# Optimization experiments

Hardware: AMD Instinct MI355X
Metric: run time of the kernel (lower is better)

Reference implementation:

```python
import jax, jax.numpy as jnp
import numpy as np

HIDDEN = 1024
HEADS = 16
HEAD_DIM = HIDDEN // HEADS  # 64
BATCH = 2
SEQ = 2048
MASK_IDENTITY = True


def setup_inputs() -> dict:
    key = jax.random.key(0)
    ks = jax.random.split(key, 9)
    s = 1.0 / np.sqrt(HIDDEN)
    return {
        "hidden_states": jax.random.normal(ks[0], (BATCH, SEQ, HIDDEN), jnp.float32),
        "Wq": jax.random.normal(ks[1], (HIDDEN, HIDDEN), jnp.float32) * s,
        "bq": jnp.zeros((HIDDEN,), jnp.float32),
        "Wk": jax.random.normal(ks[2], (HIDDEN, HIDDEN), jnp.float32) * s,
        "bk": jnp.zeros((HIDDEN,), jnp.float32),
        "Wv": jax.random.normal(ks[3], (HIDDEN, HIDDEN), jnp.float32) * s,
        "bv": jnp.zeros((HIDDEN,), jnp.float32),
        "Wd": jax.random.normal(ks[4], (HIDDEN, HIDDEN), jnp.float32) * s,
        "bd": jnp.zeros((HIDDEN,), jnp.float32),
    }


def _split_heads(x):
    # [B, S, H*Dh] -> [B, H, S, Dh]
    b, s, _ = x.shape
    return x.reshape(b, s, HEADS, HEAD_DIM).transpose(0, 2, 1, 3)


def reference(hidden_states, Wq, bq, Wk, bk, Wv, bv, Wd, bd):
    # torch Linear: y = x @ W.T + b
    q = _split_heads(hidden_states @ Wq.T + bq)  # [B,H,S,Dh]
    k = _split_heads(hidden_states @ Wk.T + bk)
    v = _split_heads(hidden_states @ Wv.T + bv)

    scores = jnp.einsum("bhqd,bhkd->bhqk", q, k) / np.sqrt(HEAD_DIM)
    if MASK_IDENTITY:
        mask_value = -jnp.finfo(scores.dtype).max
        eye = jnp.eye(scores.shape[-1], dtype=bool)  # [S,S], broadcast over B,H
        scores = jnp.where(eye, mask_value, scores)
    probs = jax.nn.softmax(scores, axis=-1)
    ctx = jnp.einsum("bhqk,bhkd->bhqd", probs, v)  # [B,H,S,Dh]
    b, h, s, d = ctx.shape
    ctx = ctx.transpose(0, 2, 1, 3).reshape(b, s, h * d)  # [B,S,H*Dh]
    return ctx @ Wd.T + bd
```

## Files before the change

kernel.cpp:

```cpp
#include <hip/hip_runtime.h>
#include <hip/hip_bf16.h>
#include <stdint.h>

#define HIDDEN 1024
#define SEQL   2048
#define NB     2
#define NH     16
#define DH     64
#define MTOT   (NB * SEQL)
#define QKVLD  3072
#define SCALE_Q 0.18033688011112042f

typedef __bf16 bf16x8 __attribute__((ext_vector_type(8)));
typedef __bf16 bf16x4 __attribute__((ext_vector_type(4)));
typedef float  f32x4  __attribute__((ext_vector_type(4)));
typedef float  f32x16 __attribute__((ext_vector_type(16)));

__device__ __forceinline__ void gload16(const void* g, void* l) {
    __builtin_amdgcn_global_load_lds(
        (const __attribute__((address_space(1))) void*)g,
        (__attribute__((address_space(3))) void*)l, 16, 0, 0);
}
__device__ __forceinline__ float exp2fast(float x) {
    float r;
    asm("v_exp_f32 %0, %1" : "=v"(r) : "v"(x));
    return r;
}
__device__ __forceinline__ unsigned cvtpk(float lo, float hi) {
    unsigned r;
    asm("v_cvt_pk_bf16_f32 %0, %1, %2" : "=v"(r) : "v"(lo), "v"(hi));
    return r;
}
__device__ __forceinline__ void pswap(unsigned& a, unsigned& b) {
    asm volatile("v_permlane32_swap_b32 %0, %1" : "+v"(a), "+v"(b));
}
__device__ __forceinline__ void barrier_vm3() {
    asm volatile("s_waitcnt vmcnt(3)" ::: "memory");
    __builtin_amdgcn_s_barrier();
    asm volatile("" ::: "memory");
}
__device__ __forceinline__ void barrier_vm4() {
    asm volatile("s_waitcnt vmcnt(4)" ::: "memory");
    __builtin_amdgcn_s_barrier();
    asm volatile("" ::: "memory");
}

__global__ void prep(const float* __restrict__ H,
                     const float* __restrict__ Wq, const float* __restrict__ Wk,
                     const float* __restrict__ Wv, const float* __restrict__ Wd,
                     const float* __restrict__ bq, const float* __restrict__ bk,
                     const float* __restrict__ bv,
                     __bf16* __restrict__ Hb, __bf16* __restrict__ Wall,
                     float* __restrict__ bqkv) {
    const int bid = blockIdx.x, tid = threadIdx.x;
    if (bid < 4096) {
        int i = bid * 256 + tid;
        float4 v = reinterpret_cast<const float4*>(H)[i];
        bf16x4 o = { (__bf16)v.x, (__bf16)v.y, (__bf16)v.z, (__bf16)v.w };
        reinterpret_cast<bf16x4*>(Hb)[i] = o;
    } else if (bid < 8192) {
        int wi = bid - 4096;
        int seg = wi >> 10;
        int i = (wi & 1023) * 256 + tid;
        const float* src = seg == 0 ? Wq : seg == 1 ? Wk : seg == 2 ? Wv : Wd;
        float sc = (seg == 0) ? SCALE_Q : 1.0f;
        float4 v = reinterpret_cast<const float4*>(src)[i];
        bf16x4 o = { (__bf16)(v.x * sc), (__bf16)(v.y * sc),
                     (__bf16)(v.z * sc), (__bf16)(v.w * sc) };
        reinterpret_cast<bf16x4*>(Wall)[(size_t)seg * 262144 + i] = o;
    } else {
        for (int i = tid; i < 3072; i += 256) {
            float v = (i < 1024) ? bq[i] * SCALE_Q
                    : (i < 2048) ? bk[i - 1024] : bv[i - 2048];
            bqkv[i] = v;
        }
    }
}

__global__ __launch_bounds__(256) void transpose_v(const __bf16* __restrict__ QKV,
                                                   __bf16* __restrict__ Vt) {
    __shared__ __bf16 t[64][66];
    const int st = blockIdx.x, bh = blockIdx.y;
    const int b = bh >> 4, h = bh & 15;
    const int tid = threadIdx.x;
    const int r = tid >> 3, c = tid & 7;
    const __bf16* src = QKV + (size_t)(b * SEQL + st * 64) * QKVLD + 2048 + h * 64;
    *(int4*)&t[r][c * 8]      = *(const int4*)(src + (size_t)r * QKVLD + c * 8);
    *(int4*)&t[r + 32][c * 8] = *(const int4*)(src + (size_t)(r + 32) * QKVLD + c * 8);
    __syncthreads();
    __bf16* dst = Vt + (size_t)bh * DH * SEQL + st * 64;
    const int d = tid >> 3;
    __bf16 tmp0[8], tmp1[8];
#pragma unroll
    for (int j = 0; j < 8; ++j) {
        tmp0[j] = t[c * 8 + j][d];
        tmp1[j] = t[c * 8 + j][d + 32];
    }
    *(int4*)(dst + (size_t)d * SEQL + c * 8)        = *(int4*)tmp0;
    *(int4*)(dst + (size_t)(d + 32) * SEQL + c * 8) = *(int4*)tmp1;
}

__global__ __launch_bounds__(256) void gemm_qkv(const __bf16* __restrict__ A,
                                                const __bf16* __restrict__ Bw,
                                                const float* __restrict__ bias,
                                                __bf16* __restrict__ C) {
    __shared__ __bf16 As[3][128 * 32];
    __shared__ __bf16 Bs[3][128 * 32];
    const int K = 1024, N = QKVLD;

    int bid = blockIdx.x;
    int swz = (bid & 7) * 96 + (bid >> 3);
    const int bm = (swz & 31) * 128;
    const int bn = (swz >> 5) * 128;

    const int tid = threadIdx.x;
    const int w = tid >> 6, l = tid & 63, g = l >> 4, lc = l & 15;
    const int wr = (w >> 1) * 64, wc = (w & 1) * 64;
    const int row = tid >> 2, ch = tid & 3;

    const __bf16* Ap = A  + (size_t)(bm + row) * K + ch * 8;
    const __bf16* Bp = Bw + (size_t)(bn + row) * K + ch * 8;

    auto gstage = [&](int kt, int slot) {
        gload16(Ap + kt,                   &As[slot][w * 512]);
        gload16(Ap + kt + (size_t)64 * K,  &As[slot][2048 + w * 512]);
        gload16(Bp + kt,                   &Bs[slot][w * 512]);
        gload16(Bp + kt + (size_t)64 * K,  &Bs[slot][2048 + w * 512]);
    };

    f32x4 acc[4][4];
    const f32x4 z4 = {0.f, 0.f, 0.f, 0.f};
#pragma unroll
    for (int i = 0; i < 4; ++i)
#pragma unroll
        for (int j = 0; j < 4; ++j) acc[i][j] = z4;

    gstage(0, 0);
    gstage(32, 1);

    for (int kt = 0, it = 0; kt < K; kt += 32, ++it) {
        barrier_vm4();
        if (kt + 64 < K) gstage(kt + 64, (it + 2) % 3);

        const __bf16* Asl = &As[it % 3][0];
        const __bf16* Bsl = &Bs[it % 3][0];
        bf16x8 af[4], bfr[4];
#pragma unroll
        for (int i = 0; i < 4; ++i)
            af[i] = *(const bf16x8*)&Asl[(wr + i * 16 + lc) * 32 + g * 8];
#pragma unroll
        for (int j = 0; j < 4; ++j)
            bfr[j] = *(const bf16x8*)&Bsl[(wc + j * 16 + lc) * 32 + g * 8];
        __builtin_amdgcn_s_setprio(1);
#pragma unroll
        for (int i = 0; i < 4; ++i)
#pragma unroll
            for (int j = 0; j < 4; ++j)
                acc[i][j] = __builtin_amdgcn_mfma_f32_16x16x32_bf16(af[i], bfr[j], acc[i][j], 0, 0, 0);
        __builtin_amdgcn_s_setprio(0);
    }

#pragma unroll
    for (int i = 0; i < 4; ++i) {
        int r0 = bm + wr + i * 16 + g * 4;
#pragma unroll
        for (int j = 0; j < 4; ++j) {
            int c = bn + wc + j * 16 + lc;
            float bb = bias[c];
#pragma unroll
            for (int r = 0; r < 4; ++r)
                C[(size_t)(r0 + r) * N + c] = (__bf16)(acc[i][j][r] + bb);
        }
    }
}

__global__ __launch_bounds__(256) void gemm_out(const __bf16* __restrict__ A,
                                                const __bf16* __restrict__ Bw,
                                                const float* __restrict__ bias,
                                                float* __restrict__ Cout) {
    __shared__ __bf16 As[3][64 * 32];
    __shared__ __bf16 Bs[3][128 * 32];
    const int K = 1024, N = 1024;

    int bid = blockIdx.x;
    int swz = (bid & 7) * 64 + (bid >> 3);
    const int bm = (swz & 63) * 64;
    const int bn = (swz >> 6) * 128;

    const int tid = threadIdx.x;
    const int w = tid >> 6, l = tid & 63, g = l >> 4, lc = l & 15;
    const int wr = (w >> 1) * 32, wc = (w & 1) * 64;
    const int row = tid >> 2, ch = tid & 3;

    const __bf16* Ap = A  + (size_t)(bm + row) * K + ch * 8;
    const __bf16* Bp = Bw + (size_t)(bn + row) * K + ch * 8;

    auto gstage = [&](int kt, int slot) {
        gload16(Ap + kt,                   &As[slot][w * 512]);
        gload16(Bp + kt,                   &Bs[slot][w * 512]);
        gload16(Bp + kt + (size_t)64 * K,  &Bs[slot][2048 + w * 512]);
    };

    f32x4 acc[2][4];
    const f32x4 z4 = {0.f, 0.f, 0.f, 0.f};
#pragma unroll
    for (int i = 0; i < 2; ++i)
#pragma unroll
        for (int j = 0; j < 4; ++j) acc[i][j] = z4;

    gstage(0, 0);
    gstage(32, 1);

    for (int kt = 0, it = 0; kt < K; kt += 32, ++it) {
        barrier_vm3();
        if (kt + 64 < K) gstage(kt + 64, (it + 2) % 3);

        const __bf16* Asl = &As[it % 3][0];
        const __bf16* Bsl = &Bs[it % 3][0];
        bf16x8 af[2], bfr[4];
#pragma unroll
        for (int i = 0; i < 2; ++i)
            af[i] = *(const bf16x8*)&Asl[(wr + i * 16 + lc) * 32 + g * 8];
#pragma unroll
        for (int j = 0; j < 4; ++j)
            bfr[j] = *(const bf16x8*)&Bsl[(wc + j * 16 + lc) * 32 + g * 8];
        __builtin_amdgcn_s_setprio(1);
#pragma unroll
        for (int i = 0; i < 2; ++i)
#pragma unroll
            for (int j = 0; j < 4; ++j)
                acc[i][j] = __builtin_amdgcn_mfma_f32_16x16x32_bf16(af[i], bfr[j], acc[i][j], 0, 0, 0);
        __builtin_amdgcn_s_setprio(0);
    }

#pragma unroll
    for (int i = 0; i < 2; ++i) {
        int r0 = bm + wr + i * 16 + g * 4;
#pragma unroll
        for (int j = 0; j < 4; ++j) {
            int c = bn + wc + j * 16 + lc;
            float bb = bias[c];
#pragma unroll
            for (int r = 0; r < 4; ++r)
                Cout[(size_t)(r0 + r) * N + c] = acc[i][j][r] + bb;
        }
    }
}

__global__ __launch_bounds__(512) void attn_kernel(const __bf16* __restrict__ QKV,
                                                   const __bf16* __restrict__ Vt,
                                                   __bf16* __restrict__ Ctx) {
    __shared__ __bf16 k_lds[3][128][64];
    __shared__ __bf16 v_lds[3][64][128];
    __shared__ float  bc[8][32];

    const int tid = threadIdx.x;
    const int w  = tid >> 6;
    const int l  = tid & 63;
    const int ql = l & 31;
    const int lh = l >> 5;

    int bid = blockIdx.x;
    int swz = (bid & 7) * 32 + (bid >> 3);
    const int qt = swz & 7, bh = swz >> 3;
    const int b = bh >> 4, hd = bh & 15;
    const int qw = qt * 256 + w * 32;

    const __bf16* Qg = QKV + (size_t)b * SEQL * QKVLD + hd * DH;
    const __bf16* Kg = Qg + 1024;
    const __bf16* Vg = Vt + (size_t)bh * DH * SEQL;

    bf16x8 qf[4];
    {
        const __bf16* qp = Qg + (size_t)(qw + ql) * QKVLD + lh * 8;
#pragma unroll
        for (int c = 0; c < 4; ++c) qf[c] = *(const bf16x8*)(qp + c * 16);
    }

    const int sr   = l >> 3;
    const int gcol = ((l & 7) ^ sr) * 8;
    const int vr  = l >> 4;
    const int vch = l & 15;
    auto stage = [&](int kb, int slot) {
        gload16(Kg + (size_t)(kb + w * 8 + sr) * QKVLD + gcol,      &k_lds[slot][w * 8][0]);
        gload16(Kg + (size_t)(kb + 64 + w * 8 + sr) * QKVLD + gcol, &k_lds[slot][64 + w * 8][0]);
        int dr0 = w * 4 + vr;
        int dr1 = 32 + w * 4 + vr;
        gload16(Vg + (size_t)dr0 * SEQL + kb + (vch ^ (dr0 & 7)) * 8, &v_lds[slot][w * 4][0]);
        gload16(Vg + (size_t)dr1 * SEQL + kb + (vch ^ (dr1 & 7)) * 8, &v_lds[slot][32 + w * 4][0]);
    };

    f32x16 o0, o1;
#pragma unroll
    for (int r = 0; r < 16; ++r) { o0[r] = 0.f; o1[r] = 0.f; }
    float l8[8];
#pragma unroll
    for (int r = 0; r < 8; ++r) l8[r] = 0.f;

    f32x16 zc;
#pragma unroll
    for (int r = 0; r < 16; ++r) zc[r] = 0.f;

    const int NT = SEQL / 128;
    const int rsw = (ql & 7) << 3;

    stage(0, 0);
    stage(128, 1);

    for (int kt = 0; kt < NT; ++kt) {
        barrier_vm4();
        if (kt + 2 < NT) stage((kt + 2) * 128, (kt + 2) % 3);

        const int buf = kt % 3;
        const int kb = kt * 128;

#pragma unroll
        for (int sub = 0; sub < 2; ++sub) {
            const int kbs = kb + sub * 64;
            const int ro  = sub * 64;

            f32x16 sA, sB;
            __builtin_amdgcn_s_setprio(1);
            {
                bf16x8 k0 = *(const bf16x8*)&k_lds[buf][ro + ql]     [(lh * 8) ^ rsw];
                bf16x8 k1 = *(const bf16x8*)&k_lds[buf][ro + 32 + ql][(lh * 8) ^ rsw];
                sA = __builtin_amdgcn_mfma_f32_32x32x16_bf16(k0, qf[0], zc, 0, 0, 0);
                sB = __builtin_amdgcn_mfma_f32_32x32x16_bf16(k1, qf[0], zc, 0, 0, 0);
            }
#pragma unroll
            for (int c = 1; c < 4; ++c) {
                bf16x8 k0 = *(const bf16x8*)&k_lds[buf][ro + ql]     [(c * 16 + lh * 8) ^ rsw];
                bf16x8 k1 = *(const bf16x8*)&k_lds[buf][ro + 32 + ql][(c * 16 + lh * 8) ^ rsw];
                sA = __builtin_amdgcn_mfma_f32_32x32x16_bf16(k0, qf[c], sA, 0, 0, 0);
                sB = __builtin_amdgcn_mfma_f32_32x32x16_bf16(k1, qf[c], sB, 0, 0, 0);
            }
            __builtin_amdgcn_s_setprio(0);

            if (kbs < qw + 32 && qw < kbs + 64) {
                const int qg = qw + ql;
#pragma unroll
                for (int i = 0; i < 16; ++i) {
                    int kg = kbs + (i & 3) + ((i >> 2) & 3) * 8 + lh * 4;
                    if (kg == qg)      sA[i] = -1e30f;
                    if (kg + 32 == qg) sB[i] = -1e30f;
                }
            }

#pragma unroll
            for (int i = 0; i < 16; ++i) sA[i] = exp2fast(sA[i]);
#pragma unroll
            for (int i = 0; i < 16; ++i) sB[i] = exp2fast(sB[i]);
#pragma unroll
            for (int i = 0; i < 8; ++i)
                l8[i] += (sA[i] + sA[i + 8]) + (sB[i] + sB[i + 8]);

            bf16x8 pa[4];
            {
                unsigned w0 = cvtpk(sA[0],  sA[1]);
                unsigned w1 = cvtpk(sA[2],  sA[3]);
                unsigned w2 = cvtpk(sA[4],  sA[5]);
                unsigned w3 = cvtpk(sA[6],  sA[7]);
                unsigned w4 = cvtpk(sA[8],  sA[9]);
                unsigned w5 = cvtpk(sA[10], sA[11]);
                unsigned w6 = cvtpk(sA[12], sA[13]);
                unsigned w7 = cvtpk(sA[14], sA[15]);
                pswap(w0, w2); pswap(w1, w3);
                pswap(w4, w6); pswap(w5, w7);
                uint4 lo4 = {w0, w1, w2, w3};
                uint4 hi4 = {w4, w5, w6, w7};
                pa[0] = *(bf16x8*)&lo4;
                pa[1] = *(bf16x8*)&hi4;
            }
            {
                unsigned w0 = cvtpk(sB[0],  sB[1]);
                unsigned w1 = cvtpk(sB[2],  sB[3]);
                unsigned w2 = cvtpk(sB[4],  sB[5]);
                unsigned w3 = cvtpk(sB[6],  sB[7]);
                unsigned w4 = cvtpk(sB[8],  sB[9]);
                unsigned w5 = cvtpk(sB[10], sB[11]);
                unsigned w6 = cvtpk(sB[12], sB[13]);
                unsigned w7 = cvtpk(sB[14], sB[15]);
                pswap(w0, w2); pswap(w1, w3);
                pswap(w4, w6); pswap(w5, w7);
                uint4 lo4 = {w0, w1, w2, w3};
                uint4 hi4 = {w4, w5, w6, w7};
                pa[2] = *(bf16x8*)&lo4;
                pa[3] = *(bf16x8*)&hi4;
            }

            __builtin_amdgcn_s_setprio(1);
#pragma unroll
            for (int s = 0; s < 2; ++s)
#pragma unroll
                for (int sl = 0; sl < 2; ++sl) {
                    const int col = sub * 64 + s * 32 + sl * 16 + lh * 8;
                    bf16x8 v0 = *(const bf16x8*)&v_lds[buf][ql]     [col ^ rsw];
                    bf16x8 v1 = *(const bf16x8*)&v_lds[buf][32 + ql][col ^ rsw];
                    o0 = __builtin_amdgcn_mfma_f32_32x32x16_bf16(pa[s * 2 + sl], v0, o0, 0, 0, 0);
                    o1 = __builtin_amdgcn_mfma_f32_32x32x16_bf16(pa[s * 2 + sl], v1, o1, 0, 0, 0);
                }
            __builtin_amdgcn_s_setprio(0);
        }
    }

    float l_r = ((l8[0] + l8[1]) + (l8[2] + l8[3]))
              + ((l8[4] + l8[5]) + (l8[6] + l8[7]));
    l_r += __shfl_xor(l_r, 32, 64);
    if (lh == 0) bc[w][ql] = 1.f / l_r;
    asm volatile("s_waitcnt lgkmcnt(0)" ::: "memory");
    __builtin_amdgcn_wave_barrier();
#pragma unroll
    for (int r = 0; r < 16; ++r) {
        int cr = (r & 3) + (r >> 2) * 8 + lh * 4;
        float iv = bc[w][cr];
        int qrow = qw + cr;
        __bf16* cp = Ctx + (size_t)(b * SEQL + qrow) * HIDDEN + hd * DH + ql;
        cp[0]  = (__bf16)(o0[r] * iv);
        cp[32] = (__bf16)(o1[r] * iv);
    }
}

extern "C" void kernel_launch(void* const* d_in, const int* in_sizes, int n_in,
                              void* d_out, int out_size, void* d_ws, size_t ws_size,
                              hipStream_t stream) {
    const float* H  = (const float*)d_in[0];
    const float* Wq = (const float*)d_in[1];
    const float* bq = (const float*)d_in[2];
    const float* Wk = (const float*)d_in[3];
    const float* bk = (const float*)d_in[4];
    const float* Wv = (const float*)d_in[5];
    const float* bv = (const float*)d_in[6];
    const float* Wd = (const float*)d_in[7];
    const float* bd = (const float*)d_in[8];
    float* out = (float*)d_out;

    char* ws = (char*)d_ws;
    const size_t MB = 1024 * 1024;
    __bf16* Hb    = (__bf16*)(ws + 0 * MB);
    __bf16* Ctx   = (__bf16*)(ws + 0 * MB);
    __bf16* Wqkvb = (__bf16*)(ws + 8 * MB);
    __bf16* Wdb   = (__bf16*)(ws + 14 * MB);
    float*  bqkv  = (float*) (ws + 16 * MB);
    __bf16* QKV   = (__bf16*)(ws + 17 * MB);
    __bf16* Vtb   = (__bf16*)(ws + 41 * MB);
    if (ws_size < 49 * MB) return;

    prep<<<8193, 256, 0, stream>>>(H, Wq, Wk, Wv, Wd, bq, bk, bv, Hb, Wqkvb, bqkv);

    gemm_qkv<<<768, 256, 0, stream>>>(Hb, Wqkvb, bqkv, QKV);

    transpose_v<<<dim3(32, 32), 256, 0, stream>>>(QKV, Vtb);

    attn_kernel<<<256, 512, 0, stream>>>(QKV, Vtb, Ctx);

    gemm_out<<<512, 256, 0, stream>>>(Ctx, Wdb, bd, out);
}
```

Baseline: 118.5 us.

## Split attention over key halves with separate merge kernel

Attention now runs in two key halves per query tile, giving twice as many blocks and writing unnormalized partial outputs and row sums. A new merge kernel adds the two partials and normalizes them. Staging also moves from a triple to a double buffer with block barriers, which cuts shared memory. The cost is an extra launch, extra global traffic for the partials, and bf16 rounding of the partial sums.

```diff
diff --git a/kernel.cpp b/kernel.cpp
--- a/kernel.cpp
+++ b/kernel.cpp
@@ -249,10 +249,11 @@
 
 __global__ __launch_bounds__(512) void attn_kernel(const __bf16* __restrict__ QKV,
                                                    const __bf16* __restrict__ Vt,
-                                                   __bf16* __restrict__ Ctx) {
-    __shared__ __bf16 k_lds[3][128][64];
-    __shared__ __bf16 v_lds[3][64][128];
-    __shared__ float  bc[8][32];
+                                                   __bf16* __restrict__ P0,
+                                                   __bf16* __restrict__ P1,
+                                                   float* __restrict__ L) {
+    __shared__ __bf16 k_lds[2][128][64];
+    __shared__ __bf16 v_lds[2][64][128];
 
     const int tid = threadIdx.x;
     const int w  = tid >> 6;
@@ -261,14 +262,18 @@
     const int lh = l >> 5;
 
     int bid = blockIdx.x;
-    int swz = (bid & 7) * 32 + (bid >> 3);
-    const int qt = swz & 7, bh = swz >> 3;
+    int swz = (bid & 7) * 64 + (bid >> 3);
+    const int split = (swz >> 8) & 1;
+    const int bh = (swz >> 3) & 31;
+    const int qt = swz & 7;
     const int b = bh >> 4, hd = bh & 15;
     const int qw = qt * 256 + w * 32;
+    const int koff = split * 1024;
 
     const __bf16* Qg = QKV + (size_t)b * SEQL * QKVLD + hd * DH;
     const __bf16* Kg = Qg + 1024;
     const __bf16* Vg = Vt + (size_t)bh * DH * SEQL;
+    __bf16* Pg = split ? P1 : P0;
 
     bf16x8 qf[4];
     {
@@ -301,18 +306,17 @@
 #pragma unroll
     for (int r = 0; r < 16; ++r) zc[r] = 0.f;
 
-    const int NT = SEQL / 128;
+    const int NT = 1024 / 128;
     const int rsw = (ql & 7) << 3;
 
-    stage(0, 0);
-    stage(128, 1);
+    stage(koff, 0);
+    __syncthreads();
 
     for (int kt = 0; kt < NT; ++kt) {
-        barrier_vm4();
-        if (kt + 2 < NT) stage((kt + 2) * 128, (kt + 2) % 3);
-
-        const int buf = kt % 3;
-        const int kb = kt * 128;
+        const int buf = kt & 1;
+        const int kb = koff + kt * 128;
+
+        if (kt + 1 < NT) stage(kb + 128, buf ^ 1);
 
 #pragma unroll
         for (int sub = 0; sub < 2; ++sub) {
@@ -401,23 +405,42 @@
                 }
             __builtin_amdgcn_s_setprio(0);
         }
+
+        __syncthreads();
     }
 
     float l_r = ((l8[0] + l8[1]) + (l8[2] + l8[3]))
               + ((l8[4] + l8[5]) + (l8[6] + l8[7]));
     l_r += __shfl_xor(l_r, 32, 64);
-    if (lh == 0) bc[w][ql] = 1.f / l_r;
-    asm volatile("s_waitcnt lgkmcnt(0)" ::: "memory");
-    __builtin_amdgcn_wave_barrier();
+    if (lh == 0) L[(size_t)split * 65536 + bh * 2048 + qw + ql] = l_r;
 #pragma unroll
     for (int r = 0; r < 16; ++r) {
         int cr = (r & 3) + (r >> 2) * 8 + lh * 4;
-        float iv = bc[w][cr];
         int qrow = qw + cr;
-        __bf16* cp = Ctx + (size_t)(b * SEQL + qrow) * HIDDEN + hd * DH + ql;
-        cp[0]  = (__bf16)(o0[r] * iv);
-        cp[32] = (__bf16)(o1[r] * iv);
-    }
+        __bf16* cp = Pg + (size_t)(b * SEQL + qrow) * HIDDEN + hd * DH + ql;
+        cp[0]  = (__bf16)o0[r];
+        cp[32] = (__bf16)o1[r];
+    }
+}
+
+__global__ __launch_bounds__(256) void attn_merge(const __bf16* __restrict__ P1,
+                                                  const float* __restrict__ L,
+                                                  __bf16* __restrict__ Ctx) {
+    int idx = blockIdx.x * 256 + threadIdx.x;
+    int e = idx * 8;
+    int row = e >> 10, col = e & 1023;
+    int q = row & (SEQL - 1), b = row >> 11, hd = col >> 6;
+    size_t li = (size_t)(b * 16 + hd) * 2048 + q;
+    float l0 = L[li];
+    float l1 = L[65536 + li];
+    float inv = 1.f / (l0 + l1);
+    bf16x8 u0 = reinterpret_cast<const bf16x8*>(Ctx)[idx];
+    bf16x8 u1 = reinterpret_cast<const bf16x8*>(P1)[idx];
+    bf16x8 o;
+#pragma unroll
+    for (int j = 0; j < 8; ++j)
+        o[j] = (__bf16)(((float)u0[j] + (float)u1[j]) * inv);
+    reinterpret_cast<bf16x8*>(Ctx)[idx] = o;
 }
 
 extern "C" void kernel_launch(void* const* d_in, const int* in_sizes, int n_in,
@@ -443,7 +466,9 @@
     float*  bqkv  = (float*) (ws + 16 * MB);
     __bf16* QKV   = (__bf16*)(ws + 17 * MB);
     __bf16* Vtb   = (__bf16*)(ws + 41 * MB);
-    if (ws_size < 49 * MB) return;
+    __bf16* P1    = (__bf16*)(ws + 49 * MB);
+    float*  L     = (float*) (ws + 57 * MB);
+    if (ws_size < 58 * MB) return;
 
     prep<<<8193, 256, 0, stream>>>(H, Wq, Wk, Wv, Wd, bq, bk, bv, Hb, Wqkvb, bqkv);
 
@@ -451,7 +476,8 @@
 
     transpose_v<<<dim3(32, 32), 256, 0, stream>>>(QKV, Vtb);
 
-    attn_kernel<<<256, 512, 0, stream>>>(QKV, Vtb, Ctx);
+    attn_kernel<<<512, 512, 0, stream>>>(QKV, Vtb, Ctx, P1, L);
+    attn_merge<<<2048, 256, 0, stream>>>(P1, L, Ctx);
 
     gemm_out<<<512, 256, 0, stream>>>(Ctx, Wdb, bd, out);
 }
```

Result: slower. 125.6 us (+6.1%).
